# Kernel tuning notes

Measured on AMD Instinct MI355X. Metric: run time of the kernel, lower is better.

The kernel has to match this reference:

```python
import jax, jax.numpy as jnp
from jax import lax
import numpy as np

B = 4096

def _conv(x, w, b):
    # x: [B,C,H,W], w: [O,I,3,3] torch OIHW layout, VALID, stride 1
    y = lax.conv_general_dilated(x, w, (1, 1), 'VALID',
                                 dimension_numbers=('NCHW', 'OIHW', 'NCHW'))
    return y + b[None, :, None, None]

def _pool2(x):
    return lax.reduce_window(x, -jnp.inf, lax.max, (1, 1, 2, 2), (1, 1, 2, 2), 'VALID')

def _lin(x, w, b):
    # torch Linear: y = x @ W^T + b, W: [out, in]
    return x @ w.T + b

def setup_inputs() -> dict:
    key = jax.random.key(0)
    ks = jax.random.split(key, 24)
    def w(k, shape, fan_in):
        return (jax.random.normal(k, shape, dtype=jnp.float32) / np.sqrt(fan_in)).astype(jnp.float32)
    inp = {
        'x':      jax.random.normal(ks[0], (B, 1, 28, 28), dtype=jnp.float32),
        'c1_w':   w(ks[1], (50, 1, 3, 3), 9),      'c1_b':  jnp.zeros((50,), jnp.float32),
        'c2_w':   w(ks[2], (50, 50, 3, 3), 450),   'c2_b':  jnp.zeros((50,), jnp.float32),
        'c3_w':   w(ks[3], (50, 50, 3, 3), 450),   'c3_b':  jnp.zeros((50,), jnp.float32),
        'l1c1_w': w(ks[4], (500, 50 * 13 * 13), 50 * 13 * 13), 'l1c1_b': jnp.zeros((500,), jnp.float32),
        'l2c1_w': w(ks[5], (10, 500), 500),        'l2c1_b': jnp.zeros((10,), jnp.float32),
        'l1c2_w': w(ks[6], (500, 50 * 5 * 5), 50 * 5 * 5),     'l1c2_b': jnp.zeros((500,), jnp.float32),
        'l2c2_w': w(ks[7], (10, 500), 500),        'l2c2_b': jnp.zeros((10,), jnp.float32),
        'l1_w':   w(ks[8], (500, 50), 50),         'l1_b':  jnp.zeros((500,), jnp.float32),
        'l2_w':   w(ks[9], (10, 500), 500),        'l2_b':  jnp.zeros((10,), jnp.float32),
        'd1_w':   w(ks[10], (2, 50 * 13 * 13), 50 * 13 * 13),  'd1_b':  jnp.zeros((2,), jnp.float32),
        'd2_w':   w(ks[11], (2, 50 * 5 * 5), 50 * 5 * 5),      'd2_b':  jnp.zeros((2,), jnp.float32),
    }
    return inp

def reference(x, c1_w, c1_b, c2_w, c2_b, c3_w, c3_b,
              l1c1_w, l1c1_b, l2c1_w, l2c1_b,
              l1c2_w, l1c2_b, l2c2_w, l2c2_b,
              l1_w, l1_b, l2_w, l2_b, d1_w, d1_b, d2_w, d2_b):
    b = x.shape[0]
    # stage 1
    h1 = _pool2(jax.nn.relu(_conv(x, c1_w, c1_b)))           # [B,50,13,13]
    f1 = h1.reshape(b, 50 * 13 * 13)
    exit1 = jnp.argmax(_lin(f1, d1_w, d1_b), axis=1) == 0     # [B] bool
    out1 = _lin(_lin(f1, l1c1_w, l1c1_b), l2c1_w, l2c1_b)     # [B,10] (no relu, as in source)
    # stage 2 (computed densely; selection below replicates the gather/scatter routing)
    h2 = _pool2(jax.nn.relu(_conv(h1, c2_w, c2_b)))          # [B,50,5,5]
    f2 = h2.reshape(b, 50 * 5 * 5)
    exit2 = jnp.argmax(_lin(f2, d2_w, d2_b), axis=1) == 0
    out2 = _lin(_lin(f2, l1c2_w, l1c2_b), l2c2_w, l2c2_b)
    # stage 3
    h3 = _pool2(jax.nn.relu(_conv(h2, c3_w, c3_b)))          # [B,50,1,1]
    f3 = h3.reshape(b, 50)
    out3 = _lin(jax.nn.relu(_lin(f3, l1_w, l1_b)), l2_w, l2_b)
    sel = jnp.where(exit1[:, None], out1, jnp.where(exit2[:, None], out2, out3))
    # original returns cat(out1_subset, out2_subset, out3_subset) + an index order;
    # we return the equivalent per-sample outputs in original batch order.
    return jax.nn.log_softmax(sel, axis=1)
```

## Files before the change

kernel.cpp:

```cpp
#include <hip/hip_runtime.h>
#include <hip/hip_bf16.h>
#include <cstdint>


typedef __bf16 bf16_t;
typedef __bf16 bf16x8 __attribute__((ext_vector_type(8)));
typedef float  f32x4  __attribute__((ext_vector_type(4)));

#define B_IMG 4096


__device__ void role_conv1(char* smem, int blk,
    const float* __restrict__ x, const float* __restrict__ w1,
    const float* __restrict__ b1, float* __restrict__ h1)
{
    float* ws = (float*)smem;
    float* bs = ws + 456;
    const int t = threadIdx.x;
    for (int i = t; i < 450; i += 256) ws[i] = w1[i];
    if (t < 50) bs[t] = b1[t];
    __syncthreads();

    const int idx = blk * 256 + t;
    if (idx >= B_IMG * 169) return;
    const int b   = idx / 169;
    const int pos = idx % 169;
    const int py = pos / 13, px = pos % 13;

    const float* xp = x + (size_t)b * 784 + (2 * py) * 28 + 2 * px;
    float p[4][4];
#pragma unroll
    for (int r = 0; r < 4; ++r)
#pragma unroll
        for (int c = 0; c < 4; ++c) p[r][c] = xp[r * 28 + c];

    float* hb = h1 + (size_t)b * 8480 + pos;
    if (pos < 30) h1[(size_t)b * 8480 + 8450 + pos] = 0.f;

    for (int oc = 0; oc < 50; ++oc) {
        const float* wp = &ws[oc * 9];
        const float w00 = wp[0], w01 = wp[1], w02 = wp[2];
        const float w10 = wp[3], w11 = wp[4], w12 = wp[5];
        const float w20 = wp[6], w21 = wp[7], w22 = wp[8];
        float a[2][2];
#pragma unroll
        for (int dy = 0; dy < 2; ++dy)
#pragma unroll
            for (int dx = 0; dx < 2; ++dx) {
                a[dy][dx] = p[dy + 0][dx + 0] * w00 + p[dy + 0][dx + 1] * w01 + p[dy + 0][dx + 2] * w02
                          + p[dy + 1][dx + 0] * w10 + p[dy + 1][dx + 1] * w11 + p[dy + 1][dx + 2] * w12
                          + p[dy + 2][dx + 0] * w20 + p[dy + 2][dx + 1] * w21 + p[dy + 2][dx + 2] * w22;
            }
        float v = fmaxf(fmaxf(a[0][0], a[0][1]), fmaxf(a[1][0], a[1][1])) + bs[oc];
        hb[oc * 169] = fmaxf(v, 0.f);
    }
}

__device__ void role_wb16(int blk, const float* __restrict__ src,
                          bf16_t* __restrict__ dst, int N, int K, int Kp, int total)
{
    const int idx = blk * 256 + threadIdx.x;
    if (idx >= total) return;
    const int n = idx / Kp, k = idx % Kp;
    const float v = (n < N && k < K) ? src[(size_t)n * K + k] : 0.f;
    dst[idx] = (bf16_t)v;
}

__device__ void role_w2t(int blk, const float* __restrict__ w2, float* __restrict__ w2p)
{
    const int idx = blk * 256 + threadIdx.x;
    if (idx >= 50 * 600) return;
    const int ic = idx / 600, r = idx % 600, oc = r / 12, j = r % 12;
    w2p[idx] = (j < 9) ? w2[oc * 450 + ic * 9 + j] : 0.f;
}

__device__ void role_conv2(char* smem, int b,
    const float* __restrict__ h1, const float* __restrict__ w2p,
    const float* __restrict__ b2, float* __restrict__ h2)
{
    float* in   = (float*)smem;
    float* wbuf = in + 8452;
    const int t = threadIdx.x;
    for (int i = t; i < 8450; i += 256) in[i] = h1[(size_t)b * 8480 + i];
    {
        const float4* src = (const float4*)w2p;
        float4* dst = (float4*)wbuf;
        for (int s = t; s < 600; s += 256) dst[s] = src[s];
    }
    __syncthreads();
    if (t < 30) h2[(size_t)b * 1280 + 1250 + t] = 0.f;

    const int ocg = t / 25;
    const int pos = t % 25;
    const int py = pos / 5, px = pos % 5;
    const int oc0 = ocg * 5;
    const bool act = (t < 250);

    float acc[5][4];
#pragma unroll
    for (int j = 0; j < 5; ++j)
#pragma unroll
        for (int q = 0; q < 4; ++q) acc[j][q] = 0.f;

    const float* ib = &in[(2 * py) * 13 + 2 * px];

    for (int ic0 = 0; ic0 < 50; ic0 += 4) {
        const int cur = (ic0 >> 2) & 1;
        if (ic0 + 4 < 50) {
            const int nxt = cur ^ 1;
            const int nic2 = (50 - ic0 - 4 < 4) ? (50 - ic0 - 4) : 4;
            const float4* src = (const float4*)(w2p + (size_t)(ic0 + 4) * 600);
            float4* dst = (float4*)(wbuf + nxt * 2400);
            for (int s = t; s < nic2 * 150; s += 256) dst[s] = src[s];
        }
        if (act) {
            const int nic = (50 - ic0 < 4) ? (50 - ic0) : 4;
            for (int icl = 0; icl < nic; ++icl) {
                const int ic = ic0 + icl;
                float p[4][4];
                const float* ip = ib + ic * 169;
#pragma unroll
                for (int r = 0; r < 4; ++r)
#pragma unroll
                    for (int c = 0; c < 4; ++c) p[r][c] = ip[r * 13 + c];
                const float* wl = wbuf + cur * 2400 + icl * 600 + oc0 * 12;
#pragma unroll
                for (int j = 0; j < 5; ++j) {
                    const f32x4 wv0 = *(const f32x4*)(wl + j * 12);
                    const f32x4 wv1 = *(const f32x4*)(wl + j * 12 + 4);
                    const f32x4 wv2 = *(const f32x4*)(wl + j * 12 + 8);
                    const float w00 = wv0[0], w01 = wv0[1], w02 = wv0[2];
                    const float w10 = wv0[3], w11 = wv1[0], w12 = wv1[1];
                    const float w20 = wv1[2], w21 = wv1[3], w22 = wv2[0];
#pragma unroll
                    for (int dy = 0; dy < 2; ++dy)
#pragma unroll
                        for (int dx = 0; dx < 2; ++dx) {
                            acc[j][dy * 2 + dx] +=
                                  p[dy + 0][dx + 0] * w00 + p[dy + 0][dx + 1] * w01 + p[dy + 0][dx + 2] * w02
                                + p[dy + 1][dx + 0] * w10 + p[dy + 1][dx + 1] * w11 + p[dy + 1][dx + 2] * w12
                                + p[dy + 2][dx + 0] * w20 + p[dy + 2][dx + 1] * w21 + p[dy + 2][dx + 2] * w22;
                        }
                }
            }
        }
        __syncthreads();
    }

    if (act) {
#pragma unroll
        for (int j = 0; j < 5; ++j) {
            float v = fmaxf(fmaxf(acc[j][0], acc[j][1]), fmaxf(acc[j][2], acc[j][3]));
            h2[(size_t)b * 1280 + (oc0 + j) * 25 + pos] = fmaxf(v + b2[oc0 + j], 0.f);
        }
    }
}

__device__ void role_conv3(char* smem, int blk,
    const float* __restrict__ h2, const float* __restrict__ w3,
    const float* __restrict__ b3, float* __restrict__ f3)
{
    float* in = (float*)smem;
    const int t = threadIdx.x;
    for (int i = t; i < 5000; i += 256) {
        const int img = i / 1250, off = i % 1250;
        in[i] = h2[(size_t)(blk * 4 + img) * 1280 + off];
    }
    __syncthreads();
    const int il = t >> 6;
    const int oc = t & 63;
    if (oc >= 50) return;

    const float* ip0 = &in[il * 1250];
    float a00 = 0.f, a01 = 0.f, a10 = 0.f, a11 = 0.f;
    for (int ic = 0; ic < 50; ++ic) {
        float p[4][4];
        const float* ip = ip0 + ic * 25;
#pragma unroll
        for (int r = 0; r < 4; ++r)
#pragma unroll
            for (int c = 0; c < 4; ++c) p[r][c] = ip[r * 5 + c];
        const float* wp = &w3[((size_t)oc * 50 + ic) * 9];
        const float w00 = wp[0], w01 = wp[1], w02 = wp[2];
        const float w10 = wp[3], w11 = wp[4], w12 = wp[5];
        const float w20 = wp[6], w21 = wp[7], w22 = wp[8];
        a00 += p[0][0]*w00 + p[0][1]*w01 + p[0][2]*w02 + p[1][0]*w10 + p[1][1]*w11 + p[1][2]*w12 + p[2][0]*w20 + p[2][1]*w21 + p[2][2]*w22;
        a01 += p[0][1]*w00 + p[0][2]*w01 + p[0][3]*w02 + p[1][1]*w10 + p[1][2]*w11 + p[1][3]*w12 + p[2][1]*w20 + p[2][2]*w21 + p[2][3]*w22;
        a10 += p[1][0]*w00 + p[1][1]*w01 + p[1][2]*w02 + p[2][0]*w10 + p[2][1]*w11 + p[2][2]*w12 + p[3][0]*w20 + p[3][1]*w21 + p[3][2]*w22;
        a11 += p[1][1]*w00 + p[1][2]*w01 + p[1][3]*w02 + p[2][1]*w10 + p[2][2]*w11 + p[2][3]*w12 + p[3][1]*w20 + p[3][2]*w21 + p[3][3]*w22;
    }
    float v = fmaxf(fmaxf(a00, a01), fmaxf(a10, a11)) + b3[oc];
    f3[(size_t)(blk * 4 + il) * 50 + oc] = fmaxf(v, 0.f);
}

__device__ void role_exit(char* smem, int b,
    const float* __restrict__ F, int ldf, int K,
    const float* __restrict__ dw, const float* __restrict__ db, int* __restrict__ e)
{
    float* r0 = (float*)smem;
    float* r1 = r0 + 256;
    const int t = threadIdx.x;
    const float* f = F + (size_t)b * ldf;
    float s0 = 0.f, s1 = 0.f;
    for (int i = t; i < K; i += 256) {
        const float v = f[i];
        s0 += v * dw[i];
        s1 += v * dw[K + i];
    }
    r0[t] = s0; r1[t] = s1;
    __syncthreads();
    for (int s = 128; s > 0; s >>= 1) {
        if (t < s) { r0[t] += r0[t + s]; r1[t] += r1[t + s]; }
        __syncthreads();
    }
    if (t == 0) e[b] = (r0[0] + db[0] >= r1[0] + db[1]) ? 1 : 0;
}

__device__ void role_gemm(char* smem, int g,
    const float* __restrict__ A, int lda, const bf16_t* __restrict__ W,
    const float* __restrict__ bias, float* __restrict__ C0, float* __restrict__ C1,
    int Kp, int khalf, int Nout, int ldc)
{
    bf16_t* As = (bf16_t*)smem;
    bf16_t* Bs = As + 128 * 40;

    const int t = threadIdx.x;
    const int m0 = (g & 31) * 128;
    const int n0 = ((g >> 5) & 7) * 64;
    const int kz = g >> 8;
    const int kbeg = kz ? khalf : 0;
    const int kend = kz ? Kp : khalf;
    float* C = kz ? C1 : C0;

    const int wave = t >> 6;
    const int lane = t & 63;
    const int wm = (wave >> 1) * 64;
    const int wn = (wave & 1) * 32;
    const int quad = lane >> 4;
    const int lr = lane & 15;

    f32x4 acc[4][2];
#pragma unroll
    for (int i = 0; i < 4; ++i)
#pragma unroll
        for (int j = 0; j < 2; ++j) acc[i][j] = (f32x4)0.f;

    const int ar = t >> 2;
    const int ac = (t & 3) * 8;

    for (int k0 = kbeg; k0 < kend; k0 += 32) {
        __syncthreads();
#pragma unroll
        for (int h = 0; h < 2; ++h) {
            const float* ap = A + (size_t)(m0 + ar + h * 64) * lda + k0 + ac;
            const float4 f0 = *(const float4*)ap;
            const float4 f1 = *(const float4*)(ap + 4);
            bf16x8 v;
            v[0] = (bf16_t)f0.x; v[1] = (bf16_t)f0.y; v[2] = (bf16_t)f0.z; v[3] = (bf16_t)f0.w;
            v[4] = (bf16_t)f1.x; v[5] = (bf16_t)f1.y; v[6] = (bf16_t)f1.z; v[7] = (bf16_t)f1.w;
            *(bf16x8*)&As[(ar + h * 64) * 40 + ac] = v;
        }
        *(uint4*)&Bs[ar * 40 + ac] = *(const uint4*)&W[(size_t)(n0 + ar) * Kp + k0 + ac];
        __syncthreads();

        bf16x8 af[4], bfr[2];
#pragma unroll
        for (int i = 0; i < 4; ++i)
            af[i] = *(const bf16x8*)&As[(wm + i * 16 + lr) * 40 + quad * 8];
#pragma unroll
        for (int j = 0; j < 2; ++j)
            bfr[j] = *(const bf16x8*)&Bs[(wn + j * 16 + lr) * 40 + quad * 8];
#pragma unroll
        for (int i = 0; i < 4; ++i)
#pragma unroll
            for (int j = 0; j < 2; ++j)
                acc[i][j] = __builtin_amdgcn_mfma_f32_16x16x32_bf16(af[i], bfr[j], acc[i][j], 0, 0, 0);
    }

#pragma unroll
    for (int j = 0; j < 2; ++j) {
        const int n = n0 + wn + j * 16 + lr;
        const float bv = (kz == 0 && n < Nout) ? bias[n] : 0.f;
#pragma unroll
        for (int i = 0; i < 4; ++i) {
            const int mrow = m0 + wm + i * 16 + quad * 4;
#pragma unroll
            for (int r = 0; r < 4; ++r)
                C[(size_t)(mrow + r) * ldc + n] = acc[i][j][r] + bv;
        }
    }
}

__device__ void role_lin10(char* smem, int blk,
    const float* __restrict__ U, const float* __restrict__ U2, int ldu,
    const float* __restrict__ W, const float* __restrict__ bias,
    float* __restrict__ out)
{
    float* red = (float*)smem;
    const int t = threadIdx.x;
    const int ks = t & 15;
    const int il = t >> 4;
    const int b  = blk * 16 + il;
    const float* u = U + (size_t)b * ldu;

    float acc[10];
#pragma unroll
    for (int o = 0; o < 10; ++o) acc[o] = 0.f;

    if (U2) {
        const float* u2 = U2 + (size_t)b * ldu;
        for (int i = 0; i < 31; ++i) {
            const int k = ks + i * 16;
            const float uv = u[k] + u2[k];
#pragma unroll
            for (int o = 0; o < 10; ++o) acc[o] += uv * W[o * 500 + k];
        }
        const int k = ks + 496;
        if (k < 500) {
            const float uv = u[k] + u2[k];
#pragma unroll
            for (int o = 0; o < 10; ++o) acc[o] += uv * W[o * 500 + k];
        }
    } else {
        for (int i = 0; i < 31; ++i) {
            const int k = ks + i * 16;
            const float uv = u[k];
#pragma unroll
            for (int o = 0; o < 10; ++o) acc[o] += uv * W[o * 500 + k];
        }
        const int k = ks + 496;
        if (k < 500) {
            const float uv = u[k];
#pragma unroll
            for (int o = 0; o < 10; ++o) acc[o] += uv * W[o * 500 + k];
        }
    }
#pragma unroll
    for (int o = 0; o < 10; ++o) red[(il * 10 + o) * 17 + ks] = acc[o];
    __syncthreads();
    if (t < 160) {
        const int il2 = t / 10, o = t - il2 * 10;
        float s = 0.f;
#pragma unroll
        for (int q = 0; q < 16; ++q) s += red[(il2 * 10 + o) * 17 + q];
        out[(size_t)(blk * 16 + il2) * 10 + o] = s + bias[o];
    }
}

__device__ void role_lin500(char* smem, int b,
    const float* __restrict__ f3, const float* __restrict__ w,
    const float* __restrict__ bias, float* __restrict__ u3)
{
    float* fs = (float*)smem;
    const int t = threadIdx.x;
    if (t < 50) fs[t] = f3[(size_t)b * 50 + t];
    __syncthreads();
    for (int o = t; o < 500; o += 256) {
        float s = 0.f;
#pragma unroll
        for (int k = 0; k < 50; ++k) s += fs[k] * w[o * 50 + k];
        u3[(size_t)b * 512 + o] = fmaxf(s + bias[o], 0.f);
    }
}


__global__ __launch_bounds__(256) void k_prep(
    const float* x, const float* c1w, const float* c1b, float* h1,
    const float* l1c1w, bf16_t* Wb1, const float* l1c2w, bf16_t* Wb2,
    const float* c2w, float* w2p)
{
    extern __shared__ char smem[];
    const int g = blockIdx.x;
    if (g < 2704)        role_conv1(smem, g, x, c1w, c1b, h1);
    else if (g < 19664)  role_wb16(g - 2704, l1c1w, Wb1, 500, 8450, 8480, 512 * 8480);
    else if (g < 22224)  role_wb16(g - 19664, l1c2w, Wb2, 500, 1250, 1280, 512 * 1280);
    else                 role_w2t(g - 22224, c2w, w2p);
}

__global__ __launch_bounds__(256) void k_stage1(
    const float* h1, const bf16_t* Wb1, const float* l1c1b, float* u, float* up,
    const float* d1w, const float* d1b, int* e1,
    const float* w2p, const float* c2b, float* h2)
{
    extern __shared__ char smem[];
    const int g = blockIdx.x;
    if (g < 512)         role_gemm(smem, g, h1, 8480, Wb1, l1c1b, u, up, 8480, 4256, 500, 512);
    else if (g < 4608)   role_conv2(smem, g - 512, h1, w2p, c2b, h2);
    else                 role_exit(smem, g - 4608, h1, 8480, 8450, d1w, d1b, e1);
}

__global__ __launch_bounds__(256) void k_stage2(
    const float* h2, const bf16_t* Wb2, const float* l1c2b, float* v, float* vp,
    const float* d2w, const float* d2b, int* e2,
    const float* c3w, const float* c3b, float* f3,
    const float* u, const float* up, const float* l2c1w, const float* l2c1b, float* out1)
{
    extern __shared__ char smem[];
    const int g = blockIdx.x;
    if (g < 512)         role_gemm(smem, g, h2, 1280, Wb2, l1c2b, v, vp, 1280, 640, 500, 512);
    else if (g < 1536)   role_conv3(smem, g - 512, h2, c3w, c3b, f3);
    else if (g < 1792)   role_lin10(smem, g - 1536, u, up, 512, l2c1w, l2c1b, out1);
    else                 role_exit(smem, g - 1792, h2, 1280, 1250, d2w, d2b, e2);
}

__global__ __launch_bounds__(256) void k_stage3a(
    const float* v, const float* vp, const float* l2c2w, const float* l2c2b, float* out2,
    const float* f3, const float* l1w, const float* l1b, float* u3)
{
    extern __shared__ char smem[];
    const int g = blockIdx.x;
    if (g < 256)         role_lin10(smem, g, v, vp, 512, l2c2w, l2c2b, out2);
    else                 role_lin500(smem, g - 256, f3, l1w, l1b, u3);
}

__global__ __launch_bounds__(256) void k_stage3b(
    const float* u3, const float* l2w, const float* l2b, float* out3)
{
    extern __shared__ char smem[];
    role_lin10(smem, blockIdx.x, u3, nullptr, 512, l2w, l2b, out3);
}

__global__ __launch_bounds__(256) void final_select(
    const int* __restrict__ e1, const int* __restrict__ e2,
    const float* __restrict__ o1, const float* __restrict__ o2,
    const float* __restrict__ o3, float* __restrict__ out)
{
    const int b = blockIdx.x * 256 + threadIdx.x;
    if (b >= B_IMG) return;
    const float* src = e1[b] ? o1 : (e2[b] ? o2 : o3);
    src += (size_t)b * 10;
    float v[10];
    float m = -3.4e38f;
#pragma unroll
    for (int o = 0; o < 10; ++o) { v[o] = src[o]; m = fmaxf(m, v[o]); }
    float s = 0.f;
#pragma unroll
    for (int o = 0; o < 10; ++o) s += expf(v[o] - m);
    const float ls = logf(s);
#pragma unroll
    for (int o = 0; o < 10; ++o) out[(size_t)b * 10 + o] = v[o] - m - ls;
}

static inline size_t align256(size_t v) { return (v + 255) & ~(size_t)255; }

extern "C" void kernel_launch(void* const* d_in, const int* in_sizes, int n_in,
                              void* d_out, int out_size, void* d_ws, size_t ws_size,
                              hipStream_t stream)
{
    const float* x     = (const float*)d_in[0];
    const float* c1w   = (const float*)d_in[1];
    const float* c1b   = (const float*)d_in[2];
    const float* c2w   = (const float*)d_in[3];
    const float* c2b   = (const float*)d_in[4];
    const float* c3w   = (const float*)d_in[5];
    const float* c3b   = (const float*)d_in[6];
    const float* l1c1w = (const float*)d_in[7];
    const float* l1c1b = (const float*)d_in[8];
    const float* l2c1w = (const float*)d_in[9];
    const float* l2c1b = (const float*)d_in[10];
    const float* l1c2w = (const float*)d_in[11];
    const float* l1c2b = (const float*)d_in[12];
    const float* l2c2w = (const float*)d_in[13];
    const float* l2c2b = (const float*)d_in[14];
    const float* l1w   = (const float*)d_in[15];
    const float* l1b   = (const float*)d_in[16];
    const float* l2w   = (const float*)d_in[17];
    const float* l2b   = (const float*)d_in[18];
    const float* d1w   = (const float*)d_in[19];
    const float* d1b   = (const float*)d_in[20];
    const float* d2w   = (const float*)d_in[21];
    const float* d2b   = (const float*)d_in[22];

    size_t off = 0;
    const size_t oWb1  = off; off = align256(off + (size_t)512 * 8480 * 2);
    const size_t oWb2  = off; off = align256(off + (size_t)512 * 1280 * 2);
    const size_t oW2P  = off; off = align256(off + (size_t)50 * 600 * 4);
    const size_t oOut1 = off; off = align256(off + (size_t)B_IMG * 10 * 4);
    const size_t oOut2 = off; off = align256(off + (size_t)B_IMG * 10 * 4);
    const size_t oOut3 = off; off = align256(off + (size_t)B_IMG * 10 * 4);
    const size_t oE1   = off; off = align256(off + (size_t)B_IMG * 4);
    const size_t oE2   = off; off = align256(off + (size_t)B_IMG * 4);
    const size_t oH1   = off; off = align256(off + (size_t)B_IMG * 8480 * 4);
    const size_t oH2   = off; off = align256(off + (size_t)B_IMG * 1280 * 4);
    const size_t oU    = off; off = align256(off + (size_t)B_IMG * 512 * 4);
    const size_t oUP   = off; off = align256(off + (size_t)B_IMG * 512 * 4);
    const size_t oF3   = off; off = align256(off + (size_t)B_IMG * 50 * 4);

    char* ws = (char*)d_ws;
    bf16_t* Wb1  = (bf16_t*)(ws + oWb1);
    bf16_t* Wb2  = (bf16_t*)(ws + oWb2);
    float*  w2p  = (float*) (ws + oW2P);
    float*  out1 = (float*) (ws + oOut1);
    float*  out2 = (float*) (ws + oOut2);
    float*  out3 = (float*) (ws + oOut3);
    int*    e1   = (int*)   (ws + oE1);
    int*    e2   = (int*)   (ws + oE2);
    float*  h1   = (float*) (ws + oH1);
    float*  h2   = (float*) (ws + oH2);
    float*  u    = (float*) (ws + oU);
    float*  up   = (float*) (ws + oUP);
    float*  f3   = (float*) (ws + oF3);
    float*  v    = h1;
    float*  vp   = h1 + (size_t)B_IMG * 512;
    float*  u3   = h1 + (size_t)B_IMG * 1024;

    float* out = (float*)d_out;

    k_prep<<<22342, 256, 2048, stream>>>(x, c1w, c1b, h1, l1c1w, Wb1, l1c2w, Wb2, c2w, w2p);
    k_stage1<<<8704, 256, 53248, stream>>>(h1, Wb1, l1c1b, u, up, d1w, d1b, e1, w2p, c2b, h2);
    k_stage2<<<5888, 256, 20000, stream>>>(h2, Wb2, l1c2b, v, vp, d2w, d2b, e2,
                                           c3w, c3b, f3, u, up, l2c1w, l2c1b, out1);
    k_stage3a<<<4352, 256, 10880, stream>>>(v, vp, l2c2w, l2c2b, out2, f3, l1w, l1b, u3);
    k_stage3b<<<256, 256, 10880, stream>>>(u3, l2w, l2b, out3);
    final_select<<<B_IMG / 256, 256, 0, stream>>>(e1, e2, out1, out2, out3, out);

    (void)in_sizes; (void)n_in; (void)out_size; (void)ws_size;
}
```

Measured before the change: 740.8 us.

## Fuse tail kernels into one and stream conv2 input channels through LDS

Three tail launches (out2 linear, per-image lin500 plus lin10 for out3, and the final select/log-softmax) become one kernel. Each block handles 16 images, keeps the 500-wide hidden activations and the out2/out3 logits in shared memory, and writes the final log-softmax directly. This removes two launches and the global round trips for u3, out2 and out3. Separately, conv2 now double-buffers 4 input channels at a time instead of staging the whole 50-channel image, cutting stage1 dynamic LDS from 53248 to 24832 bytes so more blocks fit per CU. The tail now runs only 256 blocks, each with a serial 16-image lin500 loop, which may leave the GPU underused.

```diff
diff --git a/kernel.cpp b/kernel.cpp
--- a/kernel.cpp
+++ b/kernel.cpp
@@ -79,9 +79,10 @@
     const float* __restrict__ b2, float* __restrict__ h2)
 {
     float* in   = (float*)smem;
-    float* wbuf = in + 8452;
+    float* wbuf = in + 1360;
     const int t = threadIdx.x;
-    for (int i = t; i < 8450; i += 256) in[i] = h1[(size_t)b * 8480 + i];
+
+    for (int s = t; s < 676; s += 256) in[s] = h1[(size_t)b * 8480 + s];
     {
         const float4* src = (const float4*)w2p;
         float4* dst = (float4*)wbuf;
@@ -102,23 +103,23 @@
 #pragma unroll
         for (int q = 0; q < 4; ++q) acc[j][q] = 0.f;
 
-    const float* ib = &in[(2 * py) * 13 + 2 * px];
-
     for (int ic0 = 0; ic0 < 50; ic0 += 4) {
         const int cur = (ic0 >> 2) & 1;
         if (ic0 + 4 < 50) {
             const int nxt = cur ^ 1;
             const int nic2 = (50 - ic0 - 4 < 4) ? (50 - ic0 - 4) : 4;
+            for (int s = t; s < nic2 * 169; s += 256)
+                in[nxt * 680 + s] = h1[(size_t)b * 8480 + (ic0 + 4) * 169 + s];
             const float4* src = (const float4*)(w2p + (size_t)(ic0 + 4) * 600);
             float4* dst = (float4*)(wbuf + nxt * 2400);
             for (int s = t; s < nic2 * 150; s += 256) dst[s] = src[s];
         }
         if (act) {
             const int nic = (50 - ic0 < 4) ? (50 - ic0) : 4;
+            const float* ibc = in + cur * 680 + (2 * py) * 13 + 2 * px;
             for (int icl = 0; icl < nic; ++icl) {
-                const int ic = ic0 + icl;
                 float p[4][4];
-                const float* ip = ib + ic * 169;
+                const float* ip = ibc + icl * 169;
 #pragma unroll
                 for (int r = 0; r < 4; ++r)
 #pragma unroll
@@ -347,22 +348,6 @@
     }
 }
 
-__device__ void role_lin500(char* smem, int b,
-    const float* __restrict__ f3, const float* __restrict__ w,
-    const float* __restrict__ bias, float* __restrict__ u3)
-{
-    float* fs = (float*)smem;
-    const int t = threadIdx.x;
-    if (t < 50) fs[t] = f3[(size_t)b * 50 + t];
-    __syncthreads();
-    for (int o = t; o < 500; o += 256) {
-        float s = 0.f;
-#pragma unroll
-        for (int k = 0; k < 50; ++k) s += fs[k] * w[o * 50 + k];
-        u3[(size_t)b * 512 + o] = fmaxf(s + bias[o], 0.f);
-    }
-}
-
 
 __global__ __launch_bounds__(256) void k_prep(
     const float* x, const float* c1w, const float* c1b, float* h1,
@@ -403,42 +388,123 @@
     else                 role_exit(smem, g - 1792, h2, 1280, 1250, d2w, d2b, e2);
 }
 
-__global__ __launch_bounds__(256) void k_stage3a(
-    const float* v, const float* vp, const float* l2c2w, const float* l2c2b, float* out2,
-    const float* f3, const float* l1w, const float* l1b, float* u3)
-{
-    extern __shared__ char smem[];
-    const int g = blockIdx.x;
-    if (g < 256)         role_lin10(smem, g, v, vp, 512, l2c2w, l2c2b, out2);
-    else                 role_lin500(smem, g - 256, f3, l1w, l1b, u3);
-}
-
-__global__ __launch_bounds__(256) void k_stage3b(
-    const float* u3, const float* l2w, const float* l2b, float* out3)
-{
-    extern __shared__ char smem[];
-    role_lin10(smem, blockIdx.x, u3, nullptr, 512, l2w, l2b, out3);
-}
-
-__global__ __launch_bounds__(256) void final_select(
-    const int* __restrict__ e1, const int* __restrict__ e2,
-    const float* __restrict__ o1, const float* __restrict__ o2,
-    const float* __restrict__ o3, float* __restrict__ out)
-{
-    const int b = blockIdx.x * 256 + threadIdx.x;
-    if (b >= B_IMG) return;
-    const float* src = e1[b] ? o1 : (e2[b] ? o2 : o3);
-    src += (size_t)b * 10;
-    float v[10];
-    float m = -3.4e38f;
-#pragma unroll
-    for (int o = 0; o < 10; ++o) { v[o] = src[o]; m = fmaxf(m, v[o]); }
-    float s = 0.f;
-#pragma unroll
-    for (int o = 0; o < 10; ++o) s += expf(v[o] - m);
-    const float ls = logf(s);
-#pragma unroll
-    for (int o = 0; o < 10; ++o) out[(size_t)b * 10 + o] = v[o] - m - ls;
+__global__ __launch_bounds__(256) void k_tail(
+    const float* __restrict__ v, const float* __restrict__ vp,
+    const float* __restrict__ l2c2w, const float* __restrict__ l2c2b,
+    const float* __restrict__ f3, const float* __restrict__ l1w, const float* __restrict__ l1b,
+    const float* __restrict__ l2w, const float* __restrict__ l2b,
+    const float* __restrict__ out1, const int* __restrict__ e1, const int* __restrict__ e2,
+    float* __restrict__ out)
+{
+    __shared__ float fs[800];
+    __shared__ float u3loc[8000];
+    __shared__ float red[2720];
+    __shared__ float o2loc[160];
+    __shared__ float o3loc[160];
+
+    const int t   = threadIdx.x;
+    const int blk = blockIdx.x;
+    const int ks  = t & 15;
+    const int il  = t >> 4;
+
+    for (int i = t; i < 800; i += 256) fs[i] = f3[(size_t)blk * 800 + i];
+    __syncthreads();
+
+    for (int im = 0; im < 16; ++im) {
+        for (int o = t; o < 500; o += 256) {
+            float s = 0.f;
+#pragma unroll
+            for (int k = 0; k < 50; ++k) s += fs[im * 50 + k] * l1w[o * 50 + k];
+            u3loc[im * 500 + o] = fmaxf(s + l1b[o], 0.f);
+        }
+    }
+
+    {
+        const float* uu  = v  + (size_t)(blk * 16 + il) * 512;
+        const float* uu2 = vp + (size_t)(blk * 16 + il) * 512;
+        float acc[10];
+#pragma unroll
+        for (int o = 0; o < 10; ++o) acc[o] = 0.f;
+        for (int i = 0; i < 31; ++i) {
+            const int k = ks + i * 16;
+            const float uv = uu[k] + uu2[k];
+#pragma unroll
+            for (int o = 0; o < 10; ++o) acc[o] += uv * l2c2w[o * 500 + k];
+        }
+        const int k = ks + 496;
+        if (k < 500) {
+            const float uv = uu[k] + uu2[k];
+#pragma unroll
+            for (int o = 0; o < 10; ++o) acc[o] += uv * l2c2w[o * 500 + k];
+        }
+        __syncthreads();
+#pragma unroll
+        for (int o = 0; o < 10; ++o) red[(il * 10 + o) * 17 + ks] = acc[o];
+        __syncthreads();
+        if (t < 160) {
+            const int il2 = t / 10, o = t - il2 * 10;
+            float s = 0.f;
+#pragma unroll
+            for (int q = 0; q < 16; ++q) s += red[(il2 * 10 + o) * 17 + q];
+            o2loc[t] = s + l2c2b[o];
+        }
+        __syncthreads();
+    }
+
+    {
+        const float* uu = u3loc + il * 500;
+        float acc[10];
+#pragma unroll
+        for (int o = 0; o < 10; ++o) acc[o] = 0.f;
+        for (int i = 0; i < 31; ++i) {
+            const int k = ks + i * 16;
+            const float uv = uu[k];
+#pragma unroll
+            for (int o = 0; o < 10; ++o) acc[o] += uv * l2w[o * 500 + k];
+        }
+        const int k = ks + 496;
+        if (k < 500) {
+            const float uv = uu[k];
+#pragma unroll
+            for (int o = 0; o < 10; ++o) acc[o] += uv * l2w[o * 500 + k];
+        }
+#pragma unroll
+        for (int o = 0; o < 10; ++o) red[(il * 10 + o) * 17 + ks] = acc[o];
+        __syncthreads();
+        if (t < 160) {
+            const int il2 = t / 10, o = t - il2 * 10;
+            float s = 0.f;
+#pragma unroll
+            for (int q = 0; q < 16; ++q) s += red[(il2 * 10 + o) * 17 + q];
+            o3loc[t] = s + l2b[o];
+        }
+        __syncthreads();
+    }
+
+    if (t < 16) {
+        const int b = blk * 16 + t;
+        float vv[10];
+        if (e1[b]) {
+            const float* src = out1 + (size_t)b * 10;
+#pragma unroll
+            for (int o = 0; o < 10; ++o) vv[o] = src[o];
+        } else if (e2[b]) {
+#pragma unroll
+            for (int o = 0; o < 10; ++o) vv[o] = o2loc[t * 10 + o];
+        } else {
+#pragma unroll
+            for (int o = 0; o < 10; ++o) vv[o] = o3loc[t * 10 + o];
+        }
+        float m = -3.4e38f;
+#pragma unroll
+        for (int o = 0; o < 10; ++o) m = fmaxf(m, vv[o]);
+        float s = 0.f;
+#pragma unroll
+        for (int o = 0; o < 10; ++o) s += expf(vv[o] - m);
+        const float ls = logf(s);
+#pragma unroll
+        for (int o = 0; o < 10; ++o) out[(size_t)b * 10 + o] = vv[o] - m - ls;
+    }
 }
 
 static inline size_t align256(size_t v) { return (v + 255) & ~(size_t)255; }
@@ -476,8 +542,6 @@
     const size_t oWb2  = off; off = align256(off + (size_t)512 * 1280 * 2);
     const size_t oW2P  = off; off = align256(off + (size_t)50 * 600 * 4);
     const size_t oOut1 = off; off = align256(off + (size_t)B_IMG * 10 * 4);
-    const size_t oOut2 = off; off = align256(off + (size_t)B_IMG * 10 * 4);
-    const size_t oOut3 = off; off = align256(off + (size_t)B_IMG * 10 * 4);
     const size_t oE1   = off; off = align256(off + (size_t)B_IMG * 4);
     const size_t oE2   = off; off = align256(off + (size_t)B_IMG * 4);
     const size_t oH1   = off; off = align256(off + (size_t)B_IMG * 8480 * 4);
@@ -491,8 +555,6 @@
     bf16_t* Wb2  = (bf16_t*)(ws + oWb2);
     float*  w2p  = (float*) (ws + oW2P);
     float*  out1 = (float*) (ws + oOut1);
-    float*  out2 = (float*) (ws + oOut2);
-    float*  out3 = (float*) (ws + oOut3);
     int*    e1   = (int*)   (ws + oE1);
     int*    e2   = (int*)   (ws + oE2);
     float*  h1   = (float*) (ws + oH1);
@@ -502,17 +564,15 @@
     float*  f3   = (float*) (ws + oF3);
     float*  v    = h1;
     float*  vp   = h1 + (size_t)B_IMG * 512;
-    float*  u3   = h1 + (size_t)B_IMG * 1024;
 
     float* out = (float*)d_out;
 
     k_prep<<<22342, 256, 2048, stream>>>(x, c1w, c1b, h1, l1c1w, Wb1, l1c2w, Wb2, c2w, w2p);
-    k_stage1<<<8704, 256, 53248, stream>>>(h1, Wb1, l1c1b, u, up, d1w, d1b, e1, w2p, c2b, h2);
+    k_stage1<<<8704, 256, 24832, stream>>>(h1, Wb1, l1c1b, u, up, d1w, d1b, e1, w2p, c2b, h2);
     k_stage2<<<5888, 256, 20000, stream>>>(h2, Wb2, l1c2b, v, vp, d2w, d2b, e2,
                                            c3w, c3b, f3, u, up, l2c1w, l2c1b, out1);
-    k_stage3a<<<4352, 256, 10880, stream>>>(v, vp, l2c2w, l2c2b, out2, f3, l1w, l1b, u3);
-    k_stage3b<<<256, 256, 10880, stream>>>(u3, l2w, l2b, out3);
-    final_select<<<B_IMG / 256, 256, 0, stream>>>(e1, e2, out1, out2, out3, out);
+    k_tail<<<256, 256, 0, stream>>>(v, vp, l2c2w, l2c2b, f3, l1w, l1b, l2w, l2b,
+                                    out1, e1, e2, out);
 
     (void)in_sizes; (void)n_in; (void)out_size; (void)ws_size;
 }
```

After: 733.5 us. Within noise of the previous version (-1.0%).
